# Kernel optimization log

Hardware: AMD Instinct MI355X
Metric: run time of the kernel (lower is better)

## Reference

```python
import jax, jax.numpy as jnp
import numpy as np

D = 64; B = 1024; M = 32; K = 16; L = 8
N_ENT = 200000; N_REL_VOCAB = 65; N_USERS = 100000; NKG = 65536
KG_WEIGHT = 1.0


def _normalize(x, eps=1e-12):
    n = jnp.sqrt(jnp.sum(x * x, axis=-1, keepdims=True))
    return x / jnp.maximum(n, eps)


def _forward(entity_emb, relation_emb, user_emb, gate, W_u_mlp, b_u_mlp, W_re,
             W_agg, b_agg, W_gatt, b_gatt, W_iatt, b_iatt, W_tatt, b_tatt,
             W_ih, W_hh, b_ih, b_hh,
             user_indices, ent_his_self, ent_his_nbr, rel_his,
             ent_pos_self, ent_pos_nbr, rel_pos,
             ent_neg_self, ent_neg_nbr, rel_neg,
             gb_his_self, gb_his_path, gb_pos_self, gb_pos_path,
             gb_neg_self, gb_neg_path, kg_head, kg_rel, kg_tail, kg_tail_neg):

    def gru_last(x):  # x: [N, L, D] -> final hidden [N, D] (PyTorch GRU gate order r,z,n)
        def step(h, xt):
            gi = xt @ W_ih.T + b_ih
            gh = h @ W_hh.T + b_hh
            ir, iz, in_ = jnp.split(gi, 3, axis=-1)
            hr, hz, hn = jnp.split(gh, 3, axis=-1)
            r = jax.nn.sigmoid(ir + hr)
            z = jax.nn.sigmoid(iz + hz)
            n = jnp.tanh(in_ + r * hn)
            return (1 - z) * n + z * h, None
        h0 = jnp.zeros((x.shape[0], D), x.dtype)
        hT, _ = jax.lax.scan(step, h0, jnp.swapaxes(x, 0, 1))
        return hT

    def agg_lc(self_idx, nbr_idx, rel_idx, u_em):
        # self_idx [N,1], nbr_idx/rel_idx [N,K], u_em [N,D]
        self_v = entity_emb[self_idx[:, 0]]                       # [N,D]
        nbr_v = entity_emb[nbr_idx]                               # [N,K,D]
        rel_v = relation_emb[rel_idx]                             # [N,K,D]
        nere = jnp.concatenate([nbr_v, rel_v], -1) @ W_re.T       # [N,K,D]
        u_att = jax.nn.relu(u_em @ W_tatt.T + b_tatt)             # [N,D]
        self1 = jnp.broadcast_to(self_v[:, None, :], nbr_v.shape)
        trans = jnp.tanh(jnp.concatenate([self1, nere], -1) @ W_gatt.T + b_gatt)
        att = jax.nn.softmax(jnp.sum(u_att[:, None, :] * trans, -1), axis=1)  # [N,K]
        new_v = jnp.einsum('nk,nkd->nd', att, nbr_v)
        agg = jnp.tanh(jnp.concatenate([self_v, new_v], -1) @ W_agg.T + b_agg)
        return self_v, _normalize(agg)

    def agg_gb(self_idx, path_idx):
        self_v = entity_emb[self_idx[:, 0]]
        hT = gru_last(entity_emb[path_idx])
        agg = jnp.tanh(jnp.concatenate([self_v, hT], -1) @ W_agg.T + b_agg)
        return _normalize(agg)

    def rs_att(hist, pre):  # hist [B,M,2D], pre [B,2D]
        pre_e = jnp.broadcast_to(pre[:, None, :], hist.shape)
        logits = jnp.tanh(jnp.concatenate([hist, pre_e], -1) @ W_iatt.T + b_iatt)[..., 0]
        att = jax.nn.softmax(logits, axis=1)
        return jnp.einsum('bm,bmd->bd', att, hist)

    user_g = user_emb[user_indices]                               # [B,D]
    g = jax.nn.sigmoid(gate)

    N = B * M
    u_rep = jnp.broadcast_to(user_g[:, None, :], (B, M, D)).reshape(N, D)
    self_hist, his_lc = agg_lc(ent_his_self.reshape(N, 1), ent_his_nbr.reshape(N, K),
                               rel_his.reshape(N, K), u_rep)
    his_gb = agg_gb(gb_his_self.reshape(N, 1), gb_his_path.reshape(N, L))
    item_hist = jnp.concatenate(
        [self_hist.reshape(B, M, D),
         (g * his_lc + (1 - g) * his_gb).reshape(B, M, D)], -1)   # [B,M,2D]

    def item_branch(self_idx, nbr_idx, rel_idx, gb_self, gb_path):
        self_v, lc = agg_lc(self_idx, nbr_idx, rel_idx, user_g)
        gb = agg_gb(gb_self, gb_path)
        item = jnp.concatenate([self_v, g * lc + (1 - g) * gb], -1)  # [B,2D]
        u_lc = rs_att(item_hist, item)                               # [B,2D]
        u = jax.nn.relu(jnp.concatenate([user_g, u_lc], -1) @ W_u_mlp.T + b_u_mlp)
        u = jnp.concatenate([user_g, _normalize(u)], -1)             # [B,2D]
        return jnp.sum(u * item, axis=1)

    pos_score = item_branch(ent_pos_self, ent_pos_nbr, rel_pos, gb_pos_self, gb_pos_path)
    neg_score = item_branch(ent_neg_self, ent_neg_nbr, rel_neg, gb_neg_self, gb_neg_path)
    rs_loss = -jnp.mean(jax.nn.log_sigmoid(pos_score - neg_score))

    head = entity_emb[kg_head]; rel = relation_emb[kg_rel]
    tail = entity_emb[kg_tail]; tail_ne = entity_emb[kg_tail_neg]
    nere = jnp.concatenate([tail, rel], 1) @ W_re.T
    nere_ne = jnp.concatenate([tail_ne, rel], 1) @ W_re.T
    s = jnp.sum((head - nere) ** 2, 1)
    s_ne = jnp.sum((head - nere_ne) ** 2, 1)
    kg_loss = -jnp.mean(jax.nn.log_sigmoid(s_ne - s))

    all_loss = rs_loss + KG_WEIGHT * kg_loss
    return pos_score, neg_score, all_loss


def setup_inputs() -> dict:
    key = jax.random.key(0)
    ks = iter(jax.random.split(key, 48))

    def nrm(shape, scale=0.1):
        return (scale * jax.random.normal(next(ks), shape)).astype(jnp.float32)

    def idx(shape, hi):
        return jax.random.randint(next(ks), shape, 0, hi)

    return dict(
        user_indices=idx((B,), N_USERS),
        ent_his_self=idx((B, M, 1), N_ENT),
        ent_his_nbr=idx((B, M, K), N_ENT),
        rel_his=idx((B, M, K), N_REL_VOCAB),
        ent_pos_self=idx((B, 1), N_ENT),
        ent_pos_nbr=idx((B, K), N_ENT),
        rel_pos=idx((B, K), N_REL_VOCAB),
        ent_neg_self=idx((B, 1), N_ENT),
        ent_neg_nbr=idx((B, K), N_ENT),
        rel_neg=idx((B, K), N_REL_VOCAB),
        gb_his_self=idx((B, M, 1), N_ENT),
        gb_his_path=idx((B, M, L), N_ENT),
        gb_pos_self=idx((B, 1), N_ENT),
        gb_pos_path=idx((B, L), N_ENT),
        gb_neg_self=idx((B, 1), N_ENT),
        gb_neg_path=idx((B, L), N_ENT),
        kg_head=idx((NKG,), N_ENT),
        kg_rel=idx((NKG,), N_REL_VOCAB),
        kg_tail=idx((NKG,), N_ENT),
        kg_tail_neg=idx((NKG,), N_ENT),
        entity_emb=nrm((N_ENT, D)),
        relation_emb=nrm((N_REL_VOCAB, D)),
        user_emb=nrm((N_USERS, D)),
        gate=jnp.zeros((D,), jnp.float32),
        W_u_mlp=nrm((D, 3 * D)), b_u_mlp=jnp.zeros((D,), jnp.float32),
        W_re=nrm((D, 2 * D)),
        W_agg=nrm((D, 2 * D)), b_agg=jnp.zeros((D,), jnp.float32),
        W_gatt=nrm((D, 2 * D)), b_gatt=jnp.zeros((D,), jnp.float32),
        W_iatt=nrm((1, 4 * D)), b_iatt=jnp.zeros((1,), jnp.float32),
        W_tatt=nrm((D, D)), b_tatt=jnp.zeros((D,), jnp.float32),
        W_ih=nrm((3 * D, D)), W_hh=nrm((3 * D, D)),
        b_ih=jnp.zeros((3 * D,), jnp.float32), b_hh=jnp.zeros((3 * D,), jnp.float32),
    )


def reference(user_indices, ent_his_self, ent_his_nbr, rel_his,
              ent_pos_self, ent_pos_nbr, rel_pos,
              ent_neg_self, ent_neg_nbr, rel_neg,
              gb_his_self, gb_his_path, gb_pos_self, gb_pos_path,
              gb_neg_self, gb_neg_path, kg_head, kg_rel, kg_tail, kg_tail_neg,
              entity_emb, relation_emb, user_emb, gate, W_u_mlp, b_u_mlp, W_re,
              W_agg, b_agg, W_gatt, b_gatt, W_iatt, b_iatt, W_tatt, b_tatt,
              W_ih, W_hh, b_ih, b_hh):
    return _forward(entity_emb, relation_emb, user_emb, gate, W_u_mlp, b_u_mlp, W_re,
                    W_agg, b_agg, W_gatt, b_gatt, W_iatt, b_iatt, W_tatt, b_tatt,
                    W_ih, W_hh, b_ih, b_hh,
                    user_indices, ent_his_self, ent_his_nbr, rel_his,
                    ent_pos_self, ent_pos_nbr, rel_pos,
                    ent_neg_self, ent_neg_nbr, rel_neg,
                    gb_his_self, gb_his_path, gb_pos_self, gb_pos_path,
                    gb_neg_self, gb_neg_path, kg_head, kg_rel, kg_tail, kg_tail_neg)
```

## Files before the change

### kernel.cpp

```cpp
#include <hip/hip_runtime.h>

#define DEV __device__ __forceinline__

#define Dd   64
#define Bb   1024
#define Mm   32
#define Kk   16
#define Ll   8
#define NKGk 65536
#define NH   32768
#define ROWS (NH + 2*Bb)
#define NGRU (ROWS/64)

typedef float v2f __attribute__((ext_vector_type(2)));

#define OFF_WTATT   0
#define OFF_WGS     4096
#define OFF_WCOMB   8192
#define OFF_WRE     16384
#define OFF_WAGG    24576
#define OFF_WU      32768
#define OFF_GVEC    45056
#define OFF_USERG   45120
#define OFF_UATT    110656
#define OFF_SELFH   176192
#define OFF_HISLC   2273344
#define OFF_HISGB   4370496
#define OFF_SELFPN  6467648
#define OFF_LCPN    6598720
#define OFF_GBPN    6729792
#define OFF_ULCPN   6860864
#define OFF_KGSUM   7123008
#define OFF_KGS     7123012
#define OFF_WIHP    7123072
#define OFF_WHHP    7135360
#define OFF_WAGP    7147648
#define OFF_RELC    7155840
#define OFF_RELR    7160000

DEV float4 ld4(const float* p){ return *reinterpret_cast<const float4*>(p); }
DEV void st4(float* p, const float4 v){ *reinterpret_cast<float4*>(p) = v; }

DEV float tanh_fast(float x){
  float cx = fminf(15.f, fmaxf(-15.f, x));
  float e = __expf(2.f*cx);
  return __fdividef(e - 1.f, e + 1.f);
}
DEV float sigmoid_fast(float x){ return __fdividef(1.f, 1.f + __expf(-x)); }

#define MVJ2(ACC2_, WROW_, XX_) { \
  _Pragma("unroll") for (int d4_ = 0; d4_ < 16; ++d4_){ \
    float4 w_ = *(const float4*)((WROW_) + 4*d4_); \
    ACC2_[2*d4_]   += (v2f){w_.x, w_.y}*(XX_); \
    ACC2_[2*d4_+1] += (v2f){w_.z, w_.w}*(XX_); } }

__global__ void prep1_kernel(const float* __restrict__ W_tatt, const float* __restrict__ W_gatt,
                             const float* __restrict__ W_re, const float* __restrict__ W_agg,
                             const float* __restrict__ W_u, const float* __restrict__ W_ih,
                             const float* __restrict__ W_hh, const float* __restrict__ gate,
                             float* __restrict__ ws)
{
  int g = blockIdx.x*256 + threadIdx.x;
  for (int i = g; i < 4096; i += 8192){
    int d = i >> 6, j = i & 63;
    ws[OFF_WTATT + j*64 + d] = W_tatt[i];
    ws[OFF_WGS   + j*64 + d] = W_gatt[d*128 + j];
  }
  for (int i = g; i < 8192; i += 8192){
    int j = i >> 6, d = i & 63;
    ws[OFF_WRE  + i] = W_re[d*128 + j];
    ws[OFF_WAGG + i] = W_agg[d*128 + j];
    float s = 0.f;
    for (int dp = 0; dp < 64; ++dp) s += W_gatt[d*128 + 64 + dp] * W_re[dp*128 + j];
    ws[OFF_WCOMB + i] = s;
  }
  for (int i = g; i < 12288; i += 8192){
    int j = i >> 6, d = i & 63;
    ws[OFF_WU + i] = W_u[d*192 + j];
  }
  for (int i = g; i < 12288; i += 8192){
    int jc = i / 768, r1 = i - jc*768;
    int ww = r1 / 96,  r2 = r1 - ww*96;
    int jj = r2 / 24,  r3 = r2 - jj*24;
    int gg = r3 >> 3,  oi = r3 & 7;
    int j = jc*4 + jj, o = gg*64 + ww*8 + oi;
    ws[OFF_WIHP + i] = W_ih[o*64 + j];
    ws[OFF_WHHP + i] = W_hh[o*64 + j];
  }
  for (int i = g; i < 8192; i += 8192){
    int jc = i >> 8, r1 = i & 255;
    int ww = r1 >> 5, r2 = r1 & 31;
    int jj = r2 >> 3, oi = r2 & 7;
    ws[OFF_WAGP + i] = W_agg[(ww*8 + oi)*128 + jc*4 + jj];
  }
  if (g < 64) ws[OFF_GVEC + g] = sigmoid_fast(gate[g]);
}

__global__ void prep2_kernel(const float* __restrict__ relation, float* __restrict__ ws)
{
  int i = blockIdx.x*256 + threadIdx.x;
  if (i >= 4160) return;
  int r = i >> 6, d = i & 63;
  const float* re = relation + r*64;
  float s1 = 0.f, s2 = 0.f;
  for (int j = 0; j < 64; ++j){
    s1 += ws[OFF_WCOMB + (64+j)*64 + d] * re[j];
    s2 += ws[OFF_WRE   + (64+j)*64 + d] * re[j];
  }
  ws[OFF_RELC + i] = s1;
  ws[OFF_RELR + i] = s2;
}

__global__ void user_prep_kernel(const int* __restrict__ uidx, const float* __restrict__ user_emb,
                                 const float* __restrict__ b_tatt, float* __restrict__ ws)
{
  int gid = blockIdx.x*256 + threadIdx.x;
  int b = gid >> 6, lane = gid & 63;
  long ui = uidx[b];
  float ugd = user_emb[ui*64 + lane];
  ws[OFF_USERG + b*64 + lane] = ugd;
  const float* WtT = ws + OFF_WTATT;
  float acc = b_tatt[lane];
  for (int j = 0; j < 64; ++j) acc += WtT[j*64 + lane] * __shfl(ugd, j);
  ws[OFF_UATT + b*64 + lane] = fmaxf(acc, 0.f);
}

#define GACC(AR_, AZ_, AN_, WP_, XS_) { \
  v2f xx_; xx_.x = (XS_); xx_.y = (XS_); \
  AR_[0] += (*(const v2f*)((WP_)+ 0))*xx_; AR_[1] += (*(const v2f*)((WP_)+ 2))*xx_; \
  AR_[2] += (*(const v2f*)((WP_)+ 4))*xx_; AR_[3] += (*(const v2f*)((WP_)+ 6))*xx_; \
  AZ_[0] += (*(const v2f*)((WP_)+ 8))*xx_; AZ_[1] += (*(const v2f*)((WP_)+10))*xx_; \
  AZ_[2] += (*(const v2f*)((WP_)+12))*xx_; AZ_[3] += (*(const v2f*)((WP_)+14))*xx_; \
  AN_[0] += (*(const v2f*)((WP_)+16))*xx_; AN_[1] += (*(const v2f*)((WP_)+18))*xx_; \
  AN_[2] += (*(const v2f*)((WP_)+20))*xx_; AN_[3] += (*(const v2f*)((WP_)+22))*xx_; }

#define AGACC(AG_, WP_, XS_) { \
  v2f xx_; xx_.x = (XS_); xx_.y = (XS_); \
  AG_[0] += (*(const v2f*)((WP_)+0))*xx_; AG_[1] += (*(const v2f*)((WP_)+2))*xx_; \
  AG_[2] += (*(const v2f*)((WP_)+4))*xx_; AG_[3] += (*(const v2f*)((WP_)+6))*xx_; }

__global__ __launch_bounds__(512, 4) void fused_kernel(
  const int* __restrict__ ghS, const int* __restrict__ ghP,
  const int* __restrict__ gpS, const int* __restrict__ gpP,
  const int* __restrict__ gnS, const int* __restrict__ gnP,
  const float* __restrict__ b_ih, const float* __restrict__ b_hh,
  const float* __restrict__ WIHP, const float* __restrict__ WHHP,
  const float* __restrict__ WAGP,
  float* __restrict__ outHis, float* __restrict__ outPN,
  const int* __restrict__ ahS, const int* __restrict__ ahN, const int* __restrict__ ahR,
  const int* __restrict__ apS, const int* __restrict__ apN, const int* __restrict__ apR,
  const int* __restrict__ anS, const int* __restrict__ anN, const int* __restrict__ anR,
  const float* __restrict__ b_gatt, const float* __restrict__ b_agg,
  const float* __restrict__ entity, float* __restrict__ ws)
{
  __shared__ float SH[8320];
  int tid = threadIdx.x;
  int bid = blockIdx.x;

  if (bid < NGRU){
    int rep = bid;
    float (*hb)[65] = (float(*)[65])SH;
    float (*xb)[65] = (float(*)[65])(SH + 4160);
    int w = __builtin_amdgcn_readfirstlane(tid >> 6);
    int lane = tid & 63;
    int rbase = rep*64;
    const int *sIv, *pIv; float* aO; int nb0;
    if (rbase < NH)          { sIv=ghS; pIv=ghP; aO=outHis;       nb0=rbase; }
    else if (rbase < NH+Bb)  { sIv=gpS; pIv=gpP; aO=outPN;        nb0=rbase-NH; }
    else                     { sIv=gnS; pIv=gnP; aO=outPN+65536;  nb0=rbase-NH-Bb; }
    int o0 = w*8;
    int nrow = nb0 + lane;

    int pt = pIv[nrow*8];
    int pt_next = pIv[nrow*8 + 1];
    {
      const float* ex = entity + (long)pt*64 + o0;
      float4 xa0 = ld4(ex), xc0 = ld4(ex + 4);
      st4(&xb[lane][o0], xa0);
      st4(&xb[lane][o0+4], xc0);
    }
    __syncthreads();

    #pragma unroll 1
    for (int t = 0; t < 8; ++t){
      float4 xa = {0,0,0,0}, xc = {0,0,0,0};
      if (t < 7){
        const float* ex = entity + (long)pt_next*64 + o0;
        xa = ld4(ex); xc = ld4(ex + 4);
        if (t < 6) pt_next = pIv[nrow*8 + t + 2];
      }
      v2f ar[4], az[4], ah[4];
      #pragma unroll
      for (int p = 0; p < 4; ++p){
        ar[p].x = b_ih[o0+2*p]      + b_hh[o0+2*p];
        ar[p].y = b_ih[o0+2*p+1]    + b_hh[o0+2*p+1];
        az[p].x = b_ih[64+o0+2*p]   + b_hh[64+o0+2*p];
        az[p].y = b_ih[64+o0+2*p+1] + b_hh[64+o0+2*p+1];
        ah[p].x = b_hh[128+o0+2*p];   ah[p].y = b_hh[128+o0+2*p+1];
      }
      if (t){
        #pragma unroll 2
        for (int jc = 0; jc < 16; ++jc){
          const float* wp = WHHP + (jc*8 + w)*96;
          float4 h4 = ld4(&hb[lane][4*jc]);
          GACC(ar, az, ah, wp,      h4.x);
          GACC(ar, az, ah, wp + 24, h4.y);
          GACC(ar, az, ah, wp + 48, h4.z);
          GACC(ar, az, ah, wp + 72, h4.w);
        }
      }
      v2f an[4];
      #pragma unroll
      for (int p = 0; p < 4; ++p){ an[p].x = b_ih[128+o0+2*p]; an[p].y = b_ih[128+o0+2*p+1]; }
      #pragma unroll 2
      for (int jc = 0; jc < 16; ++jc){
        const float* wp = WIHP + (jc*8 + w)*96;
        float4 x4 = ld4(&xb[lane][4*jc]);
        GACC(ar, az, an, wp,      x4.x);
        GACC(ar, az, an, wp + 24, x4.y);
        GACC(ar, az, an, wp + 48, x4.z);
        GACC(ar, az, an, wp + 72, x4.w);
      }
      float hp[8] = {0,0,0,0,0,0,0,0};
      if (t){
        float4 hv0 = ld4(&hb[lane][o0]); float4 hv1 = ld4(&hb[lane][o0+4]);
        hp[0]=hv0.x; hp[1]=hv0.y; hp[2]=hv0.z; hp[3]=hv0.w;
        hp[4]=hv1.x; hp[5]=hv1.y; hp[6]=hv1.z; hp[7]=hv1.w;
      }
      float hn[8];
      #pragma unroll
      for (int p = 0; p < 4; ++p){
        float r0 = sigmoid_fast(ar[p].x), r1 = sigmoid_fast(ar[p].y);
        float z0 = sigmoid_fast(az[p].x), z1 = sigmoid_fast(az[p].y);
        float n0 = tanh_fast(an[p].x + r0*ah[p].x);
        float n1 = tanh_fast(an[p].y + r1*ah[p].y);
        hn[2*p]   = (1.f - z0)*n0 + z0*hp[2*p];
        hn[2*p+1] = (1.f - z1)*n1 + z1*hp[2*p+1];
      }
      __syncthreads();
      float4 s0 = {hn[0],hn[1],hn[2],hn[3]}, s1 = {hn[4],hn[5],hn[6],hn[7]};
      st4(&hb[lane][o0], s0);
      st4(&hb[lane][o0+4], s1);
      if (t < 7){
        st4(&xb[lane][o0], xa);
        st4(&xb[lane][o0+4], xc);
      }
      __syncthreads();
    }

    long si = sIv[nrow];
    const float* es = entity + si*64 + o0;
    float4 aa = ld4(es), cc = ld4(es + 4);
    v2f ag[4];
    #pragma unroll
    for (int p = 0; p < 4; ++p){ ag[p].x = b_agg[o0+2*p]; ag[p].y = b_agg[o0+2*p+1]; }
    #pragma unroll 2
    for (int jc = 0; jc < 16; ++jc){
      const float* wp = WAGP + ((16+jc)*8 + w)*32;
      float4 h4 = ld4(&hb[lane][4*jc]);
      AGACC(ag, wp,      h4.x);
      AGACC(ag, wp + 8,  h4.y);
      AGACC(ag, wp + 16, h4.z);
      AGACC(ag, wp + 24, h4.w);
    }
    st4(&xb[lane][o0], aa);
    st4(&xb[lane][o0+4], cc);
    __syncthreads();
    #pragma unroll 2
    for (int jc = 0; jc < 16; ++jc){
      const float* wp = WAGP + (jc*8 + w)*32;
      float4 x4 = ld4(&xb[lane][4*jc]);
      AGACC(ag, wp,      x4.x);
      AGACC(ag, wp + 8,  x4.y);
      AGACC(ag, wp + 16, x4.z);
      AGACC(ag, wp + 24, x4.w);
    }
    {
      float4 s0 = {tanh_fast(ag[0].x), tanh_fast(ag[0].y), tanh_fast(ag[1].x), tanh_fast(ag[1].y)};
      float4 s1 = {tanh_fast(ag[2].x), tanh_fast(ag[2].y), tanh_fast(ag[3].x), tanh_fast(ag[3].y)};
      st4(&hb[lane][o0], s0);
      st4(&hb[lane][o0+4], s1);
    }
    __syncthreads();
    int q = tid & 7, r = tid >> 3;
    float4 v0 = ld4(&hb[r][q*8]);
    float4 v1 = ld4(&hb[r][q*8+4]);
    float ss = v0.x*v0.x + v0.y*v0.y + v0.z*v0.z + v0.w*v0.w
             + v1.x*v1.x + v1.y*v1.y + v1.z*v1.z + v1.w*v1.w;
    ss += __shfl_xor(ss, 1); ss += __shfl_xor(ss, 2); ss += __shfl_xor(ss, 4);
    float rn = __fdividef(1.f, fmaxf(sqrtf(ss), 1e-12f));
    int n2 = nb0 + r;
    float4 o4a = {v0.x*rn, v0.y*rn, v0.z*rn, v0.w*rn};
    float4 o4b = {v1.x*rn, v1.y*rn, v1.z*rn, v1.w*rn};
    st4(aO + (long)n2*64 + q*8,     o4a);
    st4(aO + (long)n2*64 + q*8 + 4, o4b);
    return;
  }

  float* WL = SH;
  int ablk = bid - NGRU;
  int tid2 = tid & 255;
  int sub  = tid >> 8;
  int k = tid2 & 15, rl = tid2 >> 4;
  int rbase = ablk*32;
  const int *sI, *nI, *rI; float *sO, *aO; int nb0, uhis;
  if (rbase < NH)          { sI=ahS; nI=ahN; rI=ahR; sO=ws+OFF_SELFH;        aO=ws+OFF_HISLC;       nb0=rbase;        uhis=1; }
  else if (rbase < NH+Bb)  { sI=apS; nI=apN; rI=apR; sO=ws+OFF_SELFPN;       aO=ws+OFF_LCPN;       nb0=rbase-NH;     uhis=0; }
  else                     { sI=anS; nI=anN; rI=anR; sO=ws+OFF_SELFPN+65536; aO=ws+OFF_LCPN+65536; nb0=rbase-NH-Bb;  uhis=0; }
  int n = nb0 + sub*16 + rl;
  int urow = uhis ? (n >> 5) : n;

  for (int i = tid; i < 1024; i += 512){
    st4(&WL[4*i],        ld4(ws + OFF_WCOMB + 4*i));
    st4(&WL[4096 + 4*i], ld4(ws + OFF_WGS   + 4*i));
  }

  const float* es = entity + (long)sI[n]*64;
  long nbI = nI[n*16 + k], rlI = rI[n*16 + k];
  const float* en = entity + nbI*64;

  v2f acc2[32];
  {
    const float* rt = ws + OFF_RELC + rlI*64;
    #pragma unroll
    for (int j4 = 0; j4 < 16; ++j4){
      float4 v = ld4(rt + 4*j4);
      acc2[2*j4]   = (v2f){v.x, v.y};
      acc2[2*j4+1] = (v2f){v.z, v.w};
    }
  }
  __syncthreads();

  float4 sc4 = ld4(b_gatt + k*4);
  #pragma unroll 2
  for (int j4 = 0; j4 < 16; ++j4){
    float4 s4 = ld4(es + 4*j4);
    float4 w0 = *(const float4*)&WL[4096 + (4*j4+0)*64 + k*4];
    float4 w1 = *(const float4*)&WL[4096 + (4*j4+1)*64 + k*4];
    float4 w2 = *(const float4*)&WL[4096 + (4*j4+2)*64 + k*4];
    float4 w3 = *(const float4*)&WL[4096 + (4*j4+3)*64 + k*4];
    sc4.x += w0.x*s4.x + w1.x*s4.y + w2.x*s4.z + w3.x*s4.w;
    sc4.y += w0.y*s4.x + w1.y*s4.y + w2.y*s4.z + w3.y*s4.w;
    sc4.z += w0.z*s4.x + w1.z*s4.y + w2.z*s4.z + w3.z*s4.w;
    sc4.w += w0.w*s4.x + w1.w*s4.y + w2.w*s4.z + w3.w*s4.w;
  }
  st4(sO + (long)n*64 + k*4, ld4(es + k*4));

  {
    float4 x4 = ld4(en);
    #pragma unroll 2
    for (int j4 = 0; j4 < 16; ++j4){
      float4 xn = ld4(en + 4*((j4+1) & 15));
      v2f xx0; xx0.x = x4.x; xx0.y = x4.x;
      MVJ2(acc2, &WL[(4*j4+0)*64], xx0);
      v2f xx1; xx1.x = x4.y; xx1.y = x4.y;
      MVJ2(acc2, &WL[(4*j4+1)*64], xx1);
      v2f xx2; xx2.x = x4.z; xx2.y = x4.z;
      MVJ2(acc2, &WL[(4*j4+2)*64], xx2);
      v2f xx3; xx3.x = x4.w; xx3.y = x4.w;
      MVJ2(acc2, &WL[(4*j4+3)*64], xx3);
      x4 = xn;
    }
  }

  int gl = (tid & 63) & 48;
  const float* up = ws + OFF_UATT + (long)urow*64;
  float lg = 0.f;
  #pragma unroll
  for (int j4 = 0; j4 < 16; ++j4){
    float4 u4 = ld4(up + 4*j4);
    float s0 = __shfl(sc4.x, gl + j4);
    float s1 = __shfl(sc4.y, gl + j4);
    float s2 = __shfl(sc4.z, gl + j4);
    float s3 = __shfl(sc4.w, gl + j4);
    lg += u4.x*tanh_fast(acc2[2*j4].x   + s0);
    lg += u4.y*tanh_fast(acc2[2*j4].y   + s1);
    lg += u4.z*tanh_fast(acc2[2*j4+1].x + s2);
    lg += u4.w*tanh_fast(acc2[2*j4+1].y + s3);
  }
  float mx = lg;
  mx = fmaxf(mx, __shfl_xor(mx, 1)); mx = fmaxf(mx, __shfl_xor(mx, 2));
  mx = fmaxf(mx, __shfl_xor(mx, 4)); mx = fmaxf(mx, __shfl_xor(mx, 8));
  float e = __expf(lg - mx);
  float se = e;
  se += __shfl_xor(se, 1); se += __shfl_xor(se, 2);
  se += __shfl_xor(se, 4); se += __shfl_xor(se, 8);
  float att = __fdividef(e, se);

  __syncthreads();
  for (int i = tid; i < 2048; i += 512)
    st4(&WL[4*i], ld4(ws + OFF_WAGG + 4*i));
  __syncthreads();

  float4 a4 = ld4(b_agg + k*4);
  #pragma unroll 2
  for (int j4 = 0; j4 < 16; ++j4){
    float4 s4 = ld4(es + 4*j4);
    float4 w0 = *(const float4*)&WL[(4*j4+0)*64 + k*4];
    float4 w1 = *(const float4*)&WL[(4*j4+1)*64 + k*4];
    float4 w2 = *(const float4*)&WL[(4*j4+2)*64 + k*4];
    float4 w3 = *(const float4*)&WL[(4*j4+3)*64 + k*4];
    a4.x += w0.x*s4.x + w1.x*s4.y + w2.x*s4.z + w3.x*s4.w;
    a4.y += w0.y*s4.x + w1.y*s4.y + w2.y*s4.z + w3.y*s4.w;
    a4.z += w0.z*s4.x + w1.z*s4.y + w2.z*s4.z + w3.z*s4.w;
    a4.w += w0.w*s4.x + w1.w*s4.y + w2.w*s4.z + w3.w*s4.w;
  }
  #pragma unroll 2
  for (int j4 = 0; j4 < 16; ++j4){
    float4 x4 = ld4(en + 4*j4);
    float xs[4] = {x4.x, x4.y, x4.z, x4.w};
    #pragma unroll
    for (int jj = 0; jj < 4; ++jj){
      float v = att * xs[jj];
      v += __shfl_xor(v, 1); v += __shfl_xor(v, 2);
      v += __shfl_xor(v, 4); v += __shfl_xor(v, 8);
      float4 wv = *(const float4*)&WL[(64 + 4*j4 + jj)*64 + k*4];
      a4.x += wv.x*v; a4.y += wv.y*v; a4.z += wv.z*v; a4.w += wv.w*v;
    }
  }
  float t0 = tanh_fast(a4.x), t1 = tanh_fast(a4.y), t2 = tanh_fast(a4.z), t3 = tanh_fast(a4.w);
  float ss = t0*t0 + t1*t1 + t2*t2 + t3*t3;
  ss += __shfl_xor(ss, 1); ss += __shfl_xor(ss, 2);
  ss += __shfl_xor(ss, 4); ss += __shfl_xor(ss, 8);
  float rn = __fdividef(1.f, fmaxf(sqrtf(ss), 1e-12f));
  float4 o4; o4.x = t0*rn; o4.y = t1*rn; o4.z = t2*rn; o4.w = t3*rn;
  st4(aO + (long)n*64 + k*4, o4);
}

__global__ __launch_bounds__(512, 4) void fused2_kernel(
  const int* __restrict__ kh, const int* __restrict__ kr,
  const int* __restrict__ kt, const int* __restrict__ ktn,
  const float* __restrict__ W_iatt, const float* __restrict__ b_iatt,
  const float* __restrict__ b_u,
  const float* __restrict__ entity, const float* __restrict__ relation,
  float* __restrict__ ws, float* __restrict__ out)
{
  __shared__ float WL[4096];
  int tid = threadIdx.x;
  int bid = blockIdx.x;
  int type = bid & 1, rep = bid >> 1;

  if (type == 0){
    int idx = rep*512 + tid;
    int br = idx >> 16, r = idx & 65535;
    const int* tailI = br ? ktn : kt;
    for (int i = tid; i < 1024; i += 512)
      st4(&WL[4*i], ld4(ws + OFF_WRE + 4*i));

    long rel = kr[r];
    const float* et = entity + (long)tailI[r]*64;
    v2f acc2[32];
    {
      const float* rt = ws + OFF_RELR + rel*64;
      #pragma unroll
      for (int j4 = 0; j4 < 16; ++j4){
        float4 v = ld4(rt + 4*j4);
        acc2[2*j4]   = (v2f){v.x, v.y};
        acc2[2*j4+1] = (v2f){v.z, v.w};
      }
    }
    __syncthreads();
    {
      float4 x4 = ld4(et);
      #pragma unroll 2
      for (int j4 = 0; j4 < 16; ++j4){
        float4 xn = ld4(et + 4*((j4+1) & 15));
        v2f xx0; xx0.x = x4.x; xx0.y = x4.x;
        MVJ2(acc2, &WL[(4*j4+0)*64], xx0);
        v2f xx1; xx1.x = x4.y; xx1.y = x4.y;
        MVJ2(acc2, &WL[(4*j4+1)*64], xx1);
        v2f xx2; xx2.x = x4.z; xx2.y = x4.z;
        MVJ2(acc2, &WL[(4*j4+2)*64], xx2);
        v2f xx3; xx3.x = x4.w; xx3.y = x4.w;
        MVJ2(acc2, &WL[(4*j4+3)*64], xx3);
        x4 = xn;
      }
    }
    const float* eh = entity + (long)kh[r]*64;
    float s = 0.f;
    #pragma unroll
    for (int j4 = 0; j4 < 16; ++j4){
      float4 h4 = ld4(eh + 4*j4);
      float d0 = h4.x - acc2[2*j4].x,   d1 = h4.y - acc2[2*j4].y;
      float d2 = h4.z - acc2[2*j4+1].x, d3 = h4.w - acc2[2*j4+1].y;
      s += d0*d0 + d1*d1 + d2*d2 + d3*d3;
    }
    ws[OFF_KGS + br*65536 + r] = s;
    return;
  }

  int gw = rep*8 + (tid >> 6), lane = tid & 63;
  int b = gw >> 1, br = gw & 1;
  const float* selfB = ws + OFF_SELFPN + br*65536 + b*64;
  const float* lcB   = ws + OFF_LCPN   + br*65536 + b*64;
  const float* gbB   = ws + OFF_GBPN   + br*65536 + b*64;
  const float* gvec  = ws + OFF_GVEC;
  const float* selfH = ws + OFF_SELFH;
  const float* hisLC = ws + OFF_HISLC;
  const float* hisGB = ws + OFF_HISGB;

  float gd = gvec[lane];
  float ugd = ws[OFF_USERG + b*64 + lane];
  float sv = selfB[lane], lcv = lcB[lane], gbv = gbB[lane];
  float gated = gd*lcv + (1.f - gd)*gbv;
  float part = W_iatt[128+lane]*sv + W_iatt[192+lane]*gated;
  #pragma unroll
  for (int m2 = 1; m2 < 64; m2 <<= 1) part += __shfl_xor(part, m2);
  float itemdot = part + b_iatt[0];

  int m = lane & 31, half = lane >> 5;
  long nrow = (long)(b*32 + m)*64;
  float sh = 0.f;
  if (half == 0){
    for (int j4 = 0; j4 < 16; ++j4){
      float4 h4 = ld4(selfH + nrow + 4*j4);
      float4 w4 = ld4(W_iatt + 4*j4);
      sh += w4.x*h4.x + w4.y*h4.y + w4.z*h4.z + w4.w*h4.w;
    }
  } else {
    for (int j4 = 0; j4 < 16; ++j4){
      float4 l4 = ld4(hisLC + nrow + 4*j4);
      float4 g4 = ld4(hisGB + nrow + 4*j4);
      float4 gg = ld4(gvec + 4*j4);
      float4 w4 = ld4(W_iatt + 64 + 4*j4);
      sh += w4.x*(gg.x*l4.x + (1.f-gg.x)*g4.x);
      sh += w4.y*(gg.y*l4.y + (1.f-gg.y)*g4.y);
      sh += w4.z*(gg.z*l4.z + (1.f-gg.z)*g4.z);
      sh += w4.w*(gg.w*l4.w + (1.f-gg.w)*g4.w);
    }
  }
  sh += __shfl_xor(sh, 32);
  float logit = tanh_fast(sh + itemdot);
  float mxv = logit;
  #pragma unroll
  for (int m2 = 1; m2 < 32; m2 <<= 1) mxv = fmaxf(mxv, __shfl_xor(mxv, m2));
  float e = __expf(logit - mxv);
  float se = e;
  #pragma unroll
  for (int m2 = 1; m2 < 32; m2 <<= 1) se += __shfl_xor(se, m2);
  float att = __fdividef(e, se);

  float u1 = 0.f, u2 = 0.f;
  for (int mm = 0; mm < 32; ++mm){
    float a = __shfl(att, mm);
    long nr = (long)(b*32 + mm)*64;
    float x1 = selfH[nr + lane];
    float x2 = gd*hisLC[nr + lane] + (1.f - gd)*hisGB[nr + lane];
    u1 += a*x1; u2 += a*x2;
  }

  const float* WuT = ws + OFF_WU;
  float acc = b_u[lane];
  for (int j = 0; j < 64; ++j) acc += WuT[j*64 + lane]        * __shfl(ugd, j);
  for (int j = 0; j < 64; ++j) acc += WuT[(64 + j)*64 + lane] * __shfl(u1, j);
  for (int j = 0; j < 64; ++j) acc += WuT[(128 + j)*64 + lane]* __shfl(u2, j);
  float uo = fmaxf(acc, 0.f);
  float ssv = uo*uo;
  #pragma unroll
  for (int m2 = 1; m2 < 64; m2 <<= 1) ssv += __shfl_xor(ssv, m2);
  float rn = __fdividef(1.f, fmaxf(sqrtf(ssv), 1e-12f));
  float nuo = uo*rn;
  float p = ugd*sv + nuo*gated;
  #pragma unroll
  for (int m2 = 1; m2 < 64; m2 <<= 1) p += __shfl_xor(p, m2);
  if (lane == 0) out[br*1024 + b] = p;
}

__global__ void kg_reduce_kernel(float* __restrict__ ws)
{
  int r = blockIdx.x*256 + threadIdx.x;
  float s  = ws[OFF_KGS + r];
  float sn = ws[OFF_KGS + 65536 + r];
  float dif = sn - s;
  float ls = fminf(dif, 0.f) - __logf(1.f + __expf(-fabsf(dif)));
  #pragma unroll
  for (int m2 = 1; m2 < 64; m2 <<= 1) ls += __shfl_xor(ls, m2);
  if ((threadIdx.x & 63) == 0) atomicAdd(ws + OFF_KGSUM, ls);
}

__global__ void loss_kernel(const float* __restrict__ ws, float* __restrict__ out)
{
  __shared__ float red[16];
  int t = threadIdx.x;
  float ps = out[t], ns_ = out[1024 + t];
  float dif = ps - ns_;
  float v = fminf(dif, 0.f) - __logf(1.f + __expf(-fabsf(dif)));
  #pragma unroll
  for (int m2 = 1; m2 < 64; m2 <<= 1) v += __shfl_xor(v, m2);
  if ((t & 63) == 0) red[t >> 6] = v;
  __syncthreads();
  if (t == 0){
    float s = 0.f;
    for (int i = 0; i < 16; ++i) s += red[i];
    float rs = -s * (1.f/1024.f);
    float kg = -ws[OFF_KGSUM] * (1.f/65536.f);
    out[2048] = rs + kg;
  }
}

extern "C" void kernel_launch(void* const* d_in, const int* in_sizes, int n_in,
                              void* d_out, int out_size, void* d_ws, size_t ws_size,
                              hipStream_t stream)
{
  const int* user_indices = (const int*)d_in[0];
  const int* ent_his_self = (const int*)d_in[1];
  const int* ent_his_nbr  = (const int*)d_in[2];
  const int* rel_his      = (const int*)d_in[3];
  const int* ent_pos_self = (const int*)d_in[4];
  const int* ent_pos_nbr  = (const int*)d_in[5];
  const int* rel_pos      = (const int*)d_in[6];
  const int* ent_neg_self = (const int*)d_in[7];
  const int* ent_neg_nbr  = (const int*)d_in[8];
  const int* rel_neg      = (const int*)d_in[9];
  const int* gb_his_self  = (const int*)d_in[10];
  const int* gb_his_path  = (const int*)d_in[11];
  const int* gb_pos_self  = (const int*)d_in[12];
  const int* gb_pos_path  = (const int*)d_in[13];
  const int* gb_neg_self  = (const int*)d_in[14];
  const int* gb_neg_path  = (const int*)d_in[15];
  const int* kg_head      = (const int*)d_in[16];
  const int* kg_rel       = (const int*)d_in[17];
  const int* kg_tail      = (const int*)d_in[18];
  const int* kg_tail_neg  = (const int*)d_in[19];
  const float* entity_emb   = (const float*)d_in[20];
  const float* relation_emb = (const float*)d_in[21];
  const float* user_emb     = (const float*)d_in[22];
  const float* gate         = (const float*)d_in[23];
  const float* W_u_mlp      = (const float*)d_in[24];
  const float* b_u_mlp      = (const float*)d_in[25];
  const float* W_re         = (const float*)d_in[26];
  const float* W_agg        = (const float*)d_in[27];
  const float* b_agg        = (const float*)d_in[28];
  const float* W_gatt       = (const float*)d_in[29];
  const float* b_gatt       = (const float*)d_in[30];
  const float* W_iatt       = (const float*)d_in[31];
  const float* b_iatt       = (const float*)d_in[32];
  const float* W_tatt       = (const float*)d_in[33];
  const float* b_tatt       = (const float*)d_in[34];
  const float* W_ih         = (const float*)d_in[35];
  const float* W_hh         = (const float*)d_in[36];
  const float* b_ih         = (const float*)d_in[37];
  const float* b_hh         = (const float*)d_in[38];
  float* ws  = (float*)d_ws;
  float* out = (float*)d_out;

  (void)hipMemsetAsync(ws + OFF_KGSUM, 0, sizeof(float), stream);
  prep1_kernel<<<32, 256, 0, stream>>>(W_tatt, W_gatt, W_re, W_agg, W_u_mlp, W_ih, W_hh, gate, ws);
  prep2_kernel<<<17, 256, 0, stream>>>(relation_emb, ws);
  user_prep_kernel<<<256, 256, 0, stream>>>(user_indices, user_emb, b_tatt, ws);
  fused_kernel<<<1632, 512, 0, stream>>>(
      gb_his_self, gb_his_path, gb_pos_self, gb_pos_path,
      gb_neg_self, gb_neg_path,
      b_ih, b_hh,
      ws + OFF_WIHP, ws + OFF_WHHP, ws + OFF_WAGP,
      ws + OFF_HISGB, ws + OFF_GBPN,
      ent_his_self, ent_his_nbr, rel_his,
      ent_pos_self, ent_pos_nbr, rel_pos,
      ent_neg_self, ent_neg_nbr, rel_neg,
      b_gatt, b_agg,
      entity_emb, ws);
  fused2_kernel<<<512, 512, 0, stream>>>(
      kg_head, kg_rel, kg_tail, kg_tail_neg,
      W_iatt, b_iatt, b_u_mlp,
      entity_emb, relation_emb, ws, out);
  kg_reduce_kernel<<<256, 256, 0, stream>>>(ws);
  loss_kernel<<<1, 1024, 0, stream>>>(ws, out);
}
```

Before: 598.3 us.

## Merge prep kernels and move KG scoring into fused kernel to cut launches

Combines the relation-prep and user-prep kernels into one launch, moves the KG triple scoring blocks from fused2 into the main fused kernel as extra blocks, and folds the KG loss reduction into fused2. The intent is to cut kernel launch count and let the KG scoring work overlap with the GRU and aggregation blocks instead of running in a separate launch. The KGS workspace buffer moves to the old ULCPN slot. Grid sizes and block roles are reshuffled, so correctness depends on the new block ranges lining up.

```diff
diff --git a/kernel.cpp b/kernel.cpp
--- a/kernel.cpp
+++ b/kernel.cpp
@@ -11,6 +11,8 @@
 #define NH   32768
 #define ROWS (NH + 2*Bb)
 #define NGRU (ROWS/64)
+#define NAGG (ROWS/32)
+#define NKGB 256
 
 typedef float v2f __attribute__((ext_vector_type(2)));
 
@@ -29,9 +31,8 @@
 #define OFF_SELFPN  6467648
 #define OFF_LCPN    6598720
 #define OFF_GBPN    6729792
-#define OFF_ULCPN   6860864
+#define OFF_KGS     6860864
 #define OFF_KGSUM   7123008
-#define OFF_KGS     7123012
 #define OFF_WIHP    7123072
 #define OFF_WHHP    7135360
 #define OFF_WAGP    7147648
@@ -96,25 +97,26 @@
   if (g < 64) ws[OFF_GVEC + g] = sigmoid_fast(gate[g]);
 }
 
-__global__ void prep2_kernel(const float* __restrict__ relation, float* __restrict__ ws)
+__global__ void prep2_kernel(const float* __restrict__ relation,
+                             const int* __restrict__ uidx, const float* __restrict__ user_emb,
+                             const float* __restrict__ b_tatt, float* __restrict__ ws)
 {
-  int i = blockIdx.x*256 + threadIdx.x;
-  if (i >= 4160) return;
-  int r = i >> 6, d = i & 63;
-  const float* re = relation + r*64;
-  float s1 = 0.f, s2 = 0.f;
-  for (int j = 0; j < 64; ++j){
-    s1 += ws[OFF_WCOMB + (64+j)*64 + d] * re[j];
-    s2 += ws[OFF_WRE   + (64+j)*64 + d] * re[j];
-  }
-  ws[OFF_RELC + i] = s1;
-  ws[OFF_RELR + i] = s2;
-}
-
-__global__ void user_prep_kernel(const int* __restrict__ uidx, const float* __restrict__ user_emb,
-                                 const float* __restrict__ b_tatt, float* __restrict__ ws)
-{
-  int gid = blockIdx.x*256 + threadIdx.x;
+  int bid = blockIdx.x;
+  if (bid < 17){
+    int i = bid*256 + threadIdx.x;
+    if (i >= 4160) return;
+    int r = i >> 6, d = i & 63;
+    const float* re = relation + r*64;
+    float s1 = 0.f, s2 = 0.f;
+    for (int j = 0; j < 64; ++j){
+      s1 += ws[OFF_WCOMB + (64+j)*64 + d] * re[j];
+      s2 += ws[OFF_WRE   + (64+j)*64 + d] * re[j];
+    }
+    ws[OFF_RELC + i] = s1;
+    ws[OFF_RELR + i] = s2;
+    return;
+  }
+  int gid = (bid - 17)*256 + threadIdx.x;
   int b = gid >> 6, lane = gid & 63;
   long ui = uidx[b];
   float ugd = user_emb[ui*64 + lane];
@@ -151,6 +153,8 @@
   const int* __restrict__ apS, const int* __restrict__ apN, const int* __restrict__ apR,
   const int* __restrict__ anS, const int* __restrict__ anN, const int* __restrict__ anR,
   const float* __restrict__ b_gatt, const float* __restrict__ b_agg,
+  const int* __restrict__ kh, const int* __restrict__ kr,
+  const int* __restrict__ kt, const int* __restrict__ ktn,
   const float* __restrict__ entity, float* __restrict__ ws)
 {
   __shared__ float SH[8320];
@@ -297,150 +301,141 @@
     return;
   }
 
-  float* WL = SH;
-  int ablk = bid - NGRU;
-  int tid2 = tid & 255;
-  int sub  = tid >> 8;
-  int k = tid2 & 15, rl = tid2 >> 4;
-  int rbase = ablk*32;
-  const int *sI, *nI, *rI; float *sO, *aO; int nb0, uhis;
-  if (rbase < NH)          { sI=ahS; nI=ahN; rI=ahR; sO=ws+OFF_SELFH;        aO=ws+OFF_HISLC;       nb0=rbase;        uhis=1; }
-  else if (rbase < NH+Bb)  { sI=apS; nI=apN; rI=apR; sO=ws+OFF_SELFPN;       aO=ws+OFF_LCPN;       nb0=rbase-NH;     uhis=0; }
-  else                     { sI=anS; nI=anN; rI=anR; sO=ws+OFF_SELFPN+65536; aO=ws+OFF_LCPN+65536; nb0=rbase-NH-Bb;  uhis=0; }
-  int n = nb0 + sub*16 + rl;
-  int urow = uhis ? (n >> 5) : n;
-
-  for (int i = tid; i < 1024; i += 512){
-    st4(&WL[4*i],        ld4(ws + OFF_WCOMB + 4*i));
-    st4(&WL[4096 + 4*i], ld4(ws + OFF_WGS   + 4*i));
-  }
-
-  const float* es = entity + (long)sI[n]*64;
-  long nbI = nI[n*16 + k], rlI = rI[n*16 + k];
-  const float* en = entity + nbI*64;
-
-  v2f acc2[32];
-  {
-    const float* rt = ws + OFF_RELC + rlI*64;
+  if (bid < NGRU + NAGG){
+    float* WL = SH;
+    int ablk = bid - NGRU;
+    int tid2 = tid & 255;
+    int sub  = tid >> 8;
+    int k = tid2 & 15, rl = tid2 >> 4;
+    int rbase = ablk*32;
+    const int *sI, *nI, *rI; float *sO, *aO; int nb0, uhis;
+    if (rbase < NH)          { sI=ahS; nI=ahN; rI=ahR; sO=ws+OFF_SELFH;        aO=ws+OFF_HISLC;       nb0=rbase;        uhis=1; }
+    else if (rbase < NH+Bb)  { sI=apS; nI=apN; rI=apR; sO=ws+OFF_SELFPN;       aO=ws+OFF_LCPN;       nb0=rbase-NH;     uhis=0; }
+    else                     { sI=anS; nI=anN; rI=anR; sO=ws+OFF_SELFPN+65536; aO=ws+OFF_LCPN+65536; nb0=rbase-NH-Bb;  uhis=0; }
+    int n = nb0 + sub*16 + rl;
+    int urow = uhis ? (n >> 5) : n;
+
+    for (int i = tid; i < 1024; i += 512){
+      st4(&WL[4*i],        ld4(ws + OFF_WCOMB + 4*i));
+      st4(&WL[4096 + 4*i], ld4(ws + OFF_WGS   + 4*i));
+    }
+
+    const float* es = entity + (long)sI[n]*64;
+    long nbI = nI[n*16 + k], rlI = rI[n*16 + k];
+    const float* en = entity + nbI*64;
+
+    v2f acc2[32];
+    {
+      const float* rt = ws + OFF_RELC + rlI*64;
+      #pragma unroll
+      for (int j4 = 0; j4 < 16; ++j4){
+        float4 v = ld4(rt + 4*j4);
+        acc2[2*j4]   = (v2f){v.x, v.y};
+        acc2[2*j4+1] = (v2f){v.z, v.w};
+      }
+    }
+    __syncthreads();
+
+    float4 sc4 = ld4(b_gatt + k*4);
+    #pragma unroll 2
+    for (int j4 = 0; j4 < 16; ++j4){
+      float4 s4 = ld4(es + 4*j4);
+      float4 w0 = *(const float4*)&WL[4096 + (4*j4+0)*64 + k*4];
+      float4 w1 = *(const float4*)&WL[4096 + (4*j4+1)*64 + k*4];
+      float4 w2 = *(const float4*)&WL[4096 + (4*j4+2)*64 + k*4];
+      float4 w3 = *(const float4*)&WL[4096 + (4*j4+3)*64 + k*4];
+      sc4.x += w0.x*s4.x + w1.x*s4.y + w2.x*s4.z + w3.x*s4.w;
+      sc4.y += w0.y*s4.x + w1.y*s4.y + w2.y*s4.z + w3.y*s4.w;
+      sc4.z += w0.z*s4.x + w1.z*s4.y + w2.z*s4.z + w3.z*s4.w;
+      sc4.w += w0.w*s4.x + w1.w*s4.y + w2.w*s4.z + w3.w*s4.w;
+    }
+    st4(sO + (long)n*64 + k*4, ld4(es + k*4));
+
+    {
+      float4 x4 = ld4(en);
+      #pragma unroll 2
+      for (int j4 = 0; j4 < 16; ++j4){
+        float4 xn = ld4(en + 4*((j4+1) & 15));
+        v2f xx0; xx0.x = x4.x; xx0.y = x4.x;
+        MVJ2(acc2, &WL[(4*j4+0)*64], xx0);
+        v2f xx1; xx1.x = x4.y; xx1.y = x4.y;
+        MVJ2(acc2, &WL[(4*j4+1)*64], xx1);
+        v2f xx2; xx2.x = x4.z; xx2.y = x4.z;
+        MVJ2(acc2, &WL[(4*j4+2)*64], xx2);
+        v2f xx3; xx3.x = x4.w; xx3.y = x4.w;
+        MVJ2(acc2, &WL[(4*j4+3)*64], xx3);
+        x4 = xn;
+      }
+    }
+
+    int gl = (tid & 63) & 48;
+    const float* up = ws + OFF_UATT + (long)urow*64;
+    float lg = 0.f;
     #pragma unroll
     for (int j4 = 0; j4 < 16; ++j4){
-      float4 v = ld4(rt + 4*j4);
-      acc2[2*j4]   = (v2f){v.x, v.y};
-      acc2[2*j4+1] = (v2f){v.z, v.w};
-    }
-  }
-  __syncthreads();
-
-  float4 sc4 = ld4(b_gatt + k*4);
-  #pragma unroll 2
-  for (int j4 = 0; j4 < 16; ++j4){
-    float4 s4 = ld4(es + 4*j4);
-    float4 w0 = *(const float4*)&WL[4096 + (4*j4+0)*64 + k*4];
-    float4 w1 = *(const float4*)&WL[4096 + (4*j4+1)*64 + k*4];
-    float4 w2 = *(const float4*)&WL[4096 + (4*j4+2)*64 + k*4];
-    float4 w3 = *(const float4*)&WL[4096 + (4*j4+3)*64 + k*4];
-    sc4.x += w0.x*s4.x + w1.x*s4.y + w2.x*s4.z + w3.x*s4.w;
-    sc4.y += w0.y*s4.x + w1.y*s4.y + w2.y*s4.z + w3.y*s4.w;
-    sc4.z += w0.z*s4.x + w1.z*s4.y + w2.z*s4.z + w3.z*s4.w;
-    sc4.w += w0.w*s4.x + w1.w*s4.y + w2.w*s4.z + w3.w*s4.w;
-  }
-  st4(sO + (long)n*64 + k*4, ld4(es + k*4));
-
-  {
-    float4 x4 = ld4(en);
+      float4 u4 = ld4(up + 4*j4);
+      float s0 = __shfl(sc4.x, gl + j4);
+      float s1 = __shfl(sc4.y, gl + j4);
+      float s2 = __shfl(sc4.z, gl + j4);
+      float s3 = __shfl(sc4.w, gl + j4);
+      lg += u4.x*tanh_fast(acc2[2*j4].x   + s0);
+      lg += u4.y*tanh_fast(acc2[2*j4].y   + s1);
+      lg += u4.z*tanh_fast(acc2[2*j4+1].x + s2);
+      lg += u4.w*tanh_fast(acc2[2*j4+1].y + s3);
+    }
+    float mx = lg;
+    mx = fmaxf(mx, __shfl_xor(mx, 1)); mx = fmaxf(mx, __shfl_xor(mx, 2));
+    mx = fmaxf(mx, __shfl_xor(mx, 4)); mx = fmaxf(mx, __shfl_xor(mx, 8));
+    float e = __expf(lg - mx);
+    float se = e;
+    se += __shfl_xor(se, 1); se += __shfl_xor(se, 2);
+    se += __shfl_xor(se, 4); se += __shfl_xor(se, 8);
+    float att = __fdividef(e, se);
+
+    __syncthreads();
+    for (int i = tid; i < 2048; i += 512)
+      st4(&WL[4*i], ld4(ws + OFF_WAGG + 4*i));
+    __syncthreads();
+
+    float4 a4 = ld4(b_agg + k*4);
     #pragma unroll 2
     for (int j4 = 0; j4 < 16; ++j4){
-      float4 xn = ld4(en + 4*((j4+1) & 15));
-      v2f xx0; xx0.x = x4.x; xx0.y = x4.x;
-      MVJ2(acc2, &WL[(4*j4+0)*64], xx0);
-      v2f xx1; xx1.x = x4.y; xx1.y = x4.y;
-      MVJ2(acc2, &WL[(4*j4+1)*64], xx1);
-      v2f xx2; xx2.x = x4.z; xx2.y = x4.z;
-      MVJ2(acc2, &WL[(4*j4+2)*64], xx2);
-      v2f xx3; xx3.x = x4.w; xx3.y = x4.w;
-      MVJ2(acc2, &WL[(4*j4+3)*64], xx3);
-      x4 = xn;
-    }
-  }
-
-  int gl = (tid & 63) & 48;
-  const float* up = ws + OFF_UATT + (long)urow*64;
-  float lg = 0.f;
-  #pragma unroll
-  for (int j4 = 0; j4 < 16; ++j4){
-    float4 u4 = ld4(up + 4*j4);
-    float s0 = __shfl(sc4.x, gl + j4);
-    float s1 = __shfl(sc4.y, gl + j4);
-    float s2 = __shfl(sc4.z, gl + j4);
-    float s3 = __shfl(sc4.w, gl + j4);
-    lg += u4.x*tanh_fast(acc2[2*j4].x   + s0);
-    lg += u4.y*tanh_fast(acc2[2*j4].y   + s1);
-    lg += u4.z*tanh_fast(acc2[2*j4+1].x + s2);
-    lg += u4.w*tanh_fast(acc2[2*j4+1].y + s3);
-  }
-  float mx = lg;
-  mx = fmaxf(mx, __shfl_xor(mx, 1)); mx = fmaxf(mx, __shfl_xor(mx, 2));
-  mx = fmaxf(mx, __shfl_xor(mx, 4)); mx = fmaxf(mx, __shfl_xor(mx, 8));
-  float e = __expf(lg - mx);
-  float se = e;
-  se += __shfl_xor(se, 1); se += __shfl_xor(se, 2);
-  se += __shfl_xor(se, 4); se += __shfl_xor(se, 8);
-  float att = __fdividef(e, se);
-
-  __syncthreads();
-  for (int i = tid; i < 2048; i += 512)
-    st4(&WL[4*i], ld4(ws + OFF_WAGG + 4*i));
-  __syncthreads();
-
-  float4 a4 = ld4(b_agg + k*4);
-  #pragma unroll 2
-  for (int j4 = 0; j4 < 16; ++j4){
-    float4 s4 = ld4(es + 4*j4);
-    float4 w0 = *(const float4*)&WL[(4*j4+0)*64 + k*4];
-    float4 w1 = *(const float4*)&WL[(4*j4+1)*64 + k*4];
-    float4 w2 = *(const float4*)&WL[(4*j4+2)*64 + k*4];
-    float4 w3 = *(const float4*)&WL[(4*j4+3)*64 + k*4];
-    a4.x += w0.x*s4.x + w1.x*s4.y + w2.x*s4.z + w3.x*s4.w;
-    a4.y += w0.y*s4.x + w1.y*s4.y + w2.y*s4.z + w3.y*s4.w;
-    a4.z += w0.z*s4.x + w1.z*s4.y + w2.z*s4.z + w3.z*s4.w;
-    a4.w += w0.w*s4.x + w1.w*s4.y + w2.w*s4.z + w3.w*s4.w;
-  }
-  #pragma unroll 2
-  for (int j4 = 0; j4 < 16; ++j4){
-    float4 x4 = ld4(en + 4*j4);
-    float xs[4] = {x4.x, x4.y, x4.z, x4.w};
-    #pragma unroll
-    for (int jj = 0; jj < 4; ++jj){
-      float v = att * xs[jj];
-      v += __shfl_xor(v, 1); v += __shfl_xor(v, 2);
-      v += __shfl_xor(v, 4); v += __shfl_xor(v, 8);
-      float4 wv = *(const float4*)&WL[(64 + 4*j4 + jj)*64 + k*4];
-      a4.x += wv.x*v; a4.y += wv.y*v; a4.z += wv.z*v; a4.w += wv.w*v;
-    }
-  }
-  float t0 = tanh_fast(a4.x), t1 = tanh_fast(a4.y), t2 = tanh_fast(a4.z), t3 = tanh_fast(a4.w);
-  float ss = t0*t0 + t1*t1 + t2*t2 + t3*t3;
-  ss += __shfl_xor(ss, 1); ss += __shfl_xor(ss, 2);
-  ss += __shfl_xor(ss, 4); ss += __shfl_xor(ss, 8);
-  float rn = __fdividef(1.f, fmaxf(sqrtf(ss), 1e-12f));
-  float4 o4; o4.x = t0*rn; o4.y = t1*rn; o4.z = t2*rn; o4.w = t3*rn;
-  st4(aO + (long)n*64 + k*4, o4);
-}
-
-__global__ __launch_bounds__(512, 4) void fused2_kernel(
-  const int* __restrict__ kh, const int* __restrict__ kr,
-  const int* __restrict__ kt, const int* __restrict__ ktn,
-  const float* __restrict__ W_iatt, const float* __restrict__ b_iatt,
-  const float* __restrict__ b_u,
-  const float* __restrict__ entity, const float* __restrict__ relation,
-  float* __restrict__ ws, float* __restrict__ out)
-{
-  __shared__ float WL[4096];
-  int tid = threadIdx.x;
-  int bid = blockIdx.x;
-  int type = bid & 1, rep = bid >> 1;
-
-  if (type == 0){
+      float4 s4 = ld4(es + 4*j4);
+      float4 w0 = *(const float4*)&WL[(4*j4+0)*64 + k*4];
+      float4 w1 = *(const float4*)&WL[(4*j4+1)*64 + k*4];
+      float4 w2 = *(const float4*)&WL[(4*j4+2)*64 + k*4];
+      float4 w3 = *(const float4*)&WL[(4*j4+3)*64 + k*4];
+      a4.x += w0.x*s4.x + w1.x*s4.y + w2.x*s4.z + w3.x*s4.w;
+      a4.y += w0.y*s4.x + w1.y*s4.y + w2.y*s4.z + w3.y*s4.w;
+      a4.z += w0.z*s4.x + w1.z*s4.y + w2.z*s4.z + w3.z*s4.w;
+      a4.w += w0.w*s4.x + w1.w*s4.y + w2.w*s4.z + w3.w*s4.w;
+    }
+    #pragma unroll 2
+    for (int j4 = 0; j4 < 16; ++j4){
+      float4 x4 = ld4(en + 4*j4);
+      float xs[4] = {x4.x, x4.y, x4.z, x4.w};
+      #pragma unroll
+      for (int jj = 0; jj < 4; ++jj){
+        float v = att * xs[jj];
+        v += __shfl_xor(v, 1); v += __shfl_xor(v, 2);
+        v += __shfl_xor(v, 4); v += __shfl_xor(v, 8);
+        float4 wv = *(const float4*)&WL[(64 + 4*j4 + jj)*64 + k*4];
+        a4.x += wv.x*v; a4.y += wv.y*v; a4.z += wv.z*v; a4.w += wv.w*v;
+      }
+    }
+    float t0 = tanh_fast(a4.x), t1 = tanh_fast(a4.y), t2 = tanh_fast(a4.z), t3 = tanh_fast(a4.w);
+    float ss = t0*t0 + t1*t1 + t2*t2 + t3*t3;
+    ss += __shfl_xor(ss, 1); ss += __shfl_xor(ss, 2);
+    ss += __shfl_xor(ss, 4); ss += __shfl_xor(ss, 8);
+    float rn = __fdividef(1.f, fmaxf(sqrtf(ss), 1e-12f));
+    float4 o4; o4.x = t0*rn; o4.y = t1*rn; o4.z = t2*rn; o4.w = t3*rn;
+    st4(aO + (long)n*64 + k*4, o4);
+    return;
+  }
+
+  {
+    float* WL = SH;
+    int rep = bid - NGRU - NAGG;
     int idx = rep*512 + tid;
     int br = idx >> 16, r = idx & 65535;
     const int* tailI = br ? ktn : kt;
@@ -486,10 +481,30 @@
       s += d0*d0 + d1*d1 + d2*d2 + d3*d3;
     }
     ws[OFF_KGS + br*65536 + r] = s;
+  }
+}
+
+__global__ __launch_bounds__(512, 4) void fused2_kernel(
+  const float* __restrict__ W_iatt, const float* __restrict__ b_iatt,
+  const float* __restrict__ b_u,
+  float* __restrict__ ws, float* __restrict__ out)
+{
+  int tid = threadIdx.x;
+  int bid = blockIdx.x;
+
+  if (bid >= 256){
+    int r = (bid - 256)*512 + tid;
+    float s  = ws[OFF_KGS + r];
+    float sn = ws[OFF_KGS + 65536 + r];
+    float dif = sn - s;
+    float ls = fminf(dif, 0.f) - __logf(1.f + __expf(-fabsf(dif)));
+    #pragma unroll
+    for (int m2 = 1; m2 < 64; m2 <<= 1) ls += __shfl_xor(ls, m2);
+    if ((tid & 63) == 0) atomicAdd(ws + OFF_KGSUM, ls);
     return;
   }
 
-  int gw = rep*8 + (tid >> 6), lane = tid & 63;
+  int gw = bid*8 + (tid >> 6), lane = tid & 63;
   int b = gw >> 1, br = gw & 1;
   const float* selfB = ws + OFF_SELFPN + br*65536 + b*64;
   const float* lcB   = ws + OFF_LCPN   + br*65536 + b*64;
@@ -564,18 +579,6 @@
   #pragma unroll
   for (int m2 = 1; m2 < 64; m2 <<= 1) p += __shfl_xor(p, m2);
   if (lane == 0) out[br*1024 + b] = p;
-}
-
-__global__ void kg_reduce_kernel(float* __restrict__ ws)
-{
-  int r = blockIdx.x*256 + threadIdx.x;
-  float s  = ws[OFF_KGS + r];
-  float sn = ws[OFF_KGS + 65536 + r];
-  float dif = sn - s;
-  float ls = fminf(dif, 0.f) - __logf(1.f + __expf(-fabsf(dif)));
-  #pragma unroll
-  for (int m2 = 1; m2 < 64; m2 <<= 1) ls += __shfl_xor(ls, m2);
-  if ((threadIdx.x & 63) == 0) atomicAdd(ws + OFF_KGSUM, ls);
 }
 
 __global__ void loss_kernel(const float* __restrict__ ws, float* __restrict__ out)
@@ -646,9 +649,8 @@
 
   (void)hipMemsetAsync(ws + OFF_KGSUM, 0, sizeof(float), stream);
   prep1_kernel<<<32, 256, 0, stream>>>(W_tatt, W_gatt, W_re, W_agg, W_u_mlp, W_ih, W_hh, gate, ws);
-  prep2_kernel<<<17, 256, 0, stream>>>(relation_emb, ws);
-  user_prep_kernel<<<256, 256, 0, stream>>>(user_indices, user_emb, b_tatt, ws);
-  fused_kernel<<<1632, 512, 0, stream>>>(
+  prep2_kernel<<<273, 256, 0, stream>>>(relation_emb, user_indices, user_emb, b_tatt, ws);
+  fused_kernel<<<NGRU + NAGG + NKGB, 512, 0, stream>>>(
       gb_his_self, gb_his_path, gb_pos_self, gb_pos_path,
       gb_neg_self, gb_neg_path,
       b_ih, b_hh,
@@ -658,11 +660,8 @@
       ent_pos_self, ent_pos_nbr, rel_pos,
       ent_neg_self, ent_neg_nbr, rel_neg,
       b_gatt, b_agg,
+      kg_head, kg_rel, kg_tail, kg_tail_neg,
       entity_emb, ws);
-  fused2_kernel<<<512, 512, 0, stream>>>(
-      kg_head, kg_rel, kg_tail, kg_tail_neg,
-      W_iatt, b_iatt, b_u_mlp,
-      entity_emb, relation_emb, ws, out);
-  kg_reduce_kernel<<<256, 256, 0, stream>>>(ws);
+  fused2_kernel<<<384, 512, 0, stream>>>(W_iatt, b_iatt, b_u_mlp, ws, out);
   loss_kernel<<<1, 1024, 0, stream>>>(ws, out);
 }
```

Result: slower. 616.4 us (+3.0%).
